# Kernel tuning notes

Hardware: AMD Instinct MI355X
Metric: run time of the kernel (lower is better)

The kernel has to match this reference:

```python
import jax, jax.numpy as jnp
import numpy as np

NUM_EMBEDDINGS = 8192
EMBEDDING_DIM = 64
N_VOXELS = 32768


def setup_inputs() -> dict:
    key = jax.random.key(0)
    k1, k2 = jax.random.split(key)
    z = jax.random.normal(k1, (N_VOXELS, EMBEDDING_DIM), dtype=jnp.float32)
    codebook = jax.random.normal(k2, (NUM_EMBEDDINGS, EMBEDDING_DIM), dtype=jnp.float32)
    return {"z": z, "codebook": codebook}


def reference(z, codebook):
    # Squared euclidean distances [N, K]; argmin is identical to argmin of cdist.
    # d2 = ||z||^2 - 2 z E^T + ||E||^2
    z_sq = jnp.sum(z * z, axis=1, keepdims=True)            # [N, 1]
    e_sq = jnp.sum(codebook * codebook, axis=1)              # [K]
    d2 = z_sq - 2.0 * (z @ codebook.T) + e_sq[None, :]       # [N, K]
    encoding_indices = jnp.argmin(d2, axis=1)                # [N] int

    quantized_feats = codebook[encoding_indices]             # [N, D] gather

    sg = jax.lax.stop_gradient
    commitment_loss = jnp.mean((z - sg(quantized_feats)) ** 2)
    vq_loss = jnp.mean((quantized_feats - sg(z)) ** 2)

    # Straight-through estimator
    quantized = z + sg(quantized_feats - z)                  # [N, D]

    return quantized, vq_loss, commitment_loss, encoding_indices
```

## Files before the change

### kernel.cpp

```cpp
#include <hip/hip_runtime.h>
#include <math.h>

#define N_VOX 32768
#define N_EMB 8192
#define DIM 64
#define NCHUNK 8
#define CODES_PER_CHUNK (N_EMB / NCHUNK)
#define TILES_PER_CHUNK (CODES_PER_CHUNK / 32)
#define NTILES (N_EMB / 32)
#define TILE_BYTES 8192
#define CHUNK_BYTES (TILES_PER_CHUNK * TILE_BYTES)

typedef _Float16 half8 __attribute__((ext_vector_type(8)));
typedef float floatx16 __attribute__((ext_vector_type(16)));

#define FP16_MIN_NORMAL 6.1035156e-5f
#define LO_SCALE 2048.0f

__global__ __launch_bounds__(64) void cbprep_kernel(const float* __restrict__ cb,
                                                    char* __restrict__ stream,
                                                    float* __restrict__ c0arr) {
    int l    = threadIdx.x;
    int m    = l & 31;
    int kg   = l >> 5;
    int tile = blockIdx.x;
    char* tbase = stream + (size_t)tile * TILE_BYTES;
    int code = tile * 32 + m;

    float ss = 0.f;
    #pragma unroll
    for (int o = 0; o < 4; ++o) {
        const float* p = cb + (size_t)code * DIM + o * 16 + kg * 8;
        half8 h, lo;
        #pragma unroll
        for (int j = 0; j < 8; ++j) {
            float x = p[j];
            ss = fmaf(x, x, ss);
            _Float16 hi = (_Float16)x;
            float hf = (float)hi;
            if (fabsf(hf) < FP16_MIN_NORMAL) { hi = (_Float16)0.f; hf = 0.f; }
            h[j]  = hi;
            lo[j] = (_Float16)((x - hf) * LO_SCALE);
        }
        *(half8*)(tbase +        o * 1024 + l * 16) = h;
        *(half8*)(tbase + 4096 + o * 1024 + l * 16) = lo;
    }
    ss += __shfl_xor(ss, 32, 64);
    if (kg == 0)
        c0arr[code] = -1024.0f * ss;
}

__global__ __launch_bounds__(512) void scan_kernel(const float* __restrict__ z,
                                                   const char* __restrict__ stream,
                                                   const float* __restrict__ c0arr,
                                                   float* __restrict__ cand_val,
                                                   int* __restrict__ cand_idx) {
    __shared__ __align__(16) char lds[2 * TILE_BYTES];
    int tid   = threadIdx.x;
    int l     = tid & 63;
    int w     = tid >> 6;
    int chunk = blockIdx.x & (NCHUNK - 1);
    int rg    = blockIdx.x >> 3;
    int m     = l & 31;
    int kg    = l >> 5;
    int rowBase = rg * 256 + w * 32;

    half8 zh[4], zl[4], zhs[4];
    const float* zrow = z + (size_t)(rowBase + m) * DIM + kg * 8;
    #pragma unroll
    for (int o = 0; o < 4; ++o) {
        const float* p = zrow + o * 16;
        #pragma unroll
        for (int j = 0; j < 8; ++j) {
            float x = p[j];
            _Float16 hi = (_Float16)x;
            float hf = (float)hi;
            if (fabsf(hf) < FP16_MIN_NORMAL) { hi = (_Float16)0.f; hf = 0.f; }
            zh[o][j] = hi;
            zl[o][j] = (_Float16)((x - hf) * LO_SCALE);
        }
        zhs[o] = zh[o] * (_Float16)2048.0f;
    }

    const char*  sbase = stream + (size_t)chunk * CHUNK_BYTES;
    const float* c0p   = c0arr + chunk * CODES_PER_CHUNK;

    float best[16];
    int   bt[16];
    #pragma unroll
    for (int i = 0; i < 16; ++i) { best[i] = -3.4e38f; bt[i] = 0; }

#define STAGE(gt, lb)                                                              \
    do {                                                                           \
        const char* _g = (gt) + w * 1024 + l * 16;                                 \
        char*       _d = (lb) + w * 1024 + l * 16;                                 \
        __builtin_amdgcn_global_load_lds(                                          \
            (const __attribute__((address_space(1))) void*)_g,                     \
            (__attribute__((address_space(3))) void*)_d, 16, 0, 0);                \
    } while (0)

    STAGE(sbase, lds);
    float c0 = c0p[m];
    __syncthreads();

    for (int t = 0; t < TILES_PER_CHUNK; ++t) {
        if (t + 1 < TILES_PER_CHUNK)
            STAGE(sbase + (size_t)(t + 1) * TILE_BYTES, lds + ((t + 1) & 1) * TILE_BYTES);
        float c0n = (t + 1 < TILES_PER_CHUNK) ? c0p[(t + 1) * 32 + m] : 0.f;

        const char* lb = lds + (t & 1) * TILE_BYTES;
        half8 bh[4], bl[4];
        #pragma unroll
        for (int o = 0; o < 4; ++o) {
            bh[o] = *(const half8*)(lb +        o * 1024 + l * 16);
            bl[o] = *(const half8*)(lb + 4096 + o * 1024 + l * 16);
        }

        floatx16 acc;
        #pragma unroll
        for (int i = 0; i < 16; ++i) acc[i] = c0;
        #pragma unroll
        for (int o = 0; o < 4; ++o) {
            acc = __builtin_amdgcn_mfma_f32_32x32x16_f16(zhs[o], bh[o], acc, 0, 0, 0);
            acc = __builtin_amdgcn_mfma_f32_32x32x16_f16(zl[o],  bh[o], acc, 0, 0, 0);
            acc = __builtin_amdgcn_mfma_f32_32x32x16_f16(zh[o],  bl[o], acc, 0, 0, 0);
        }
        #pragma unroll
        for (int i = 0; i < 16; ++i)
            if (acc[i] > best[i]) { best[i] = acc[i]; bt[i] = t; }

        c0 = c0n;
        __syncthreads();
    }
#undef STAGE

    #pragma unroll
    for (int i = 0; i < 16; ++i) {
        float v  = best[i];
        int   id = bt[i] * 32 + m;
        #pragma unroll
        for (int off = 1; off < 32; off <<= 1) {
            float ov = __shfl_xor(v, off, 64);
            int   oi = __shfl_xor(id, off, 64);
            if (ov > v || (ov == v && oi < id)) { v = ov; id = oi; }
        }
        if (m == 0) {
            int row = rowBase + (i & 3) + 8 * (i >> 2) + 4 * kg;
            cand_val[chunk * N_VOX + row] = v;
            cand_idx[chunk * N_VOX + row] = chunk * CODES_PER_CHUNK + id;
        }
    }
}

__global__ __launch_bounds__(256) void finalize_kernel(const float* __restrict__ z,
                                                       const float* __restrict__ cb,
                                                       const float* __restrict__ cand_val,
                                                       const int* __restrict__ cand_idx,
                                                       float* __restrict__ out,
                                                       float* __restrict__ partials) {
    int g    = blockIdx.x * 256 + threadIdx.x;
    int row  = g >> 3;
    int c    = g & 7;

    float v  = cand_val[c * N_VOX + row];
    int   id = cand_idx[c * N_VOX + row];
    #pragma unroll
    for (int off = 1; off < 8; off <<= 1) {
        float ov = __shfl_xor(v, off, 8);
        int   oi = __shfl_xor(id, off, 8);
        if (ov > v || (ov == v && oi < id)) { v = ov; id = oi; }
    }

    if (c == 0)
        out[(size_t)N_VOX * DIM + 2 + row] = (float)id;

    const float4* zp = (const float4*)(z  + (size_t)row * DIM + c * 8);
    const float4* qp = (const float4*)(cb + (size_t)id  * DIM + c * 8);
    float4*       op = (float4*)(out + (size_t)row * DIM + c * 8);
    float ss = 0.f;
    #pragma unroll
    for (int d = 0; d < 2; ++d) {
        float4 zt = zp[d], qt = qp[d];
        float dx = qt.x - zt.x, dy = qt.y - zt.y;
        float dz = qt.z - zt.z, dw = qt.w - zt.w;
        float4 o;
        o.x = zt.x + dx; o.y = zt.y + dy;
        o.z = zt.z + dz; o.w = zt.w + dw;
        op[d] = o;
        ss += dx*dx + dy*dy + dz*dz + dw*dw;
    }

    __shared__ float red[256];
    red[threadIdx.x] = ss;
    __syncthreads();
    #pragma unroll
    for (int s = 128; s > 0; s >>= 1) {
        if (threadIdx.x < s) red[threadIdx.x] += red[threadIdx.x + s];
        __syncthreads();
    }
    if (threadIdx.x == 0) partials[blockIdx.x] = red[0];
}

__global__ __launch_bounds__(256) void loss_kernel(const float* __restrict__ partials,
                                                   float* __restrict__ out) {
    __shared__ float red[256];
    red[threadIdx.x] = (partials[threadIdx.x]       + partials[threadIdx.x + 256])
                     + (partials[threadIdx.x + 512] + partials[threadIdx.x + 768]);
    __syncthreads();
    #pragma unroll
    for (int st = 128; st > 0; st >>= 1) {
        if (threadIdx.x < st) red[threadIdx.x] += red[threadIdx.x + st];
        __syncthreads();
    }
    if (threadIdx.x == 0) {
        float mean = red[0] / (float)((size_t)N_VOX * DIM);
        out[(size_t)N_VOX * DIM + 0] = mean;
        out[(size_t)N_VOX * DIM + 1] = mean;
    }
}

extern "C" void kernel_launch(void* const* d_in, const int* in_sizes, int n_in,
                              void* d_out, int out_size, void* d_ws, size_t ws_size,
                              hipStream_t stream) {
    const float* z  = (const float*)d_in[0];
    const float* cb = (const float*)d_in[1];
    float* out = (float*)d_out;

    char*  bstream  = (char*)d_ws;
    float* c0arr    = (float*)(bstream + (size_t)NTILES * TILE_BYTES);
    float* cand_val = c0arr + N_EMB;
    int*   cand_idx = (int*)(cand_val + (size_t)NCHUNK * N_VOX);
    float* partials = (float*)(cand_idx + (size_t)NCHUNK * N_VOX);

    cbprep_kernel  <<<dim3(NTILES), dim3(64), 0, stream>>>(cb, bstream, c0arr);
    scan_kernel    <<<dim3((N_VOX / 256) * NCHUNK), dim3(512), 0, stream>>>(z, bstream, c0arr, cand_val, cand_idx);
    finalize_kernel<<<dim3(N_VOX * 8 / 256), dim3(256), 0, stream>>>(z, cb, cand_val, cand_idx, out, partials);
    loss_kernel    <<<1, 256, 0, stream>>>(partials, out);
}
```

Measured before the change: 178.0 us.

## Fuse finalize and loss into scan via atomic winners and last-block reduction

Replaces the per-chunk candidate arrays and the separate finalize and loss kernels with a packed 64-bit atomicMax per row. The last chunk block to finish a row group, detected through a counter, gathers the code vectors, writes the outputs and accumulates the loss. A final done counter lets the last block write the mean loss. This removes two kernel launches and the candidate round trip through memory, but adds a memset, global atomics, and a tail done by only 128 blocks.

```diff
diff --git a/kernel.cpp b/kernel.cpp
--- a/kernel.cpp
+++ b/kernel.cpp
@@ -10,6 +10,7 @@
 #define NTILES (N_EMB / 32)
 #define TILE_BYTES 8192
 #define CHUNK_BYTES (TILES_PER_CHUNK * TILE_BYTES)
+#define NRG (N_VOX / 256)
 
 typedef _Float16 half8 __attribute__((ext_vector_type(8)));
 typedef float floatx16 __attribute__((ext_vector_type(16)));
@@ -51,11 +52,16 @@
 }
 
 __global__ __launch_bounds__(512) void scan_kernel(const float* __restrict__ z,
+                                                   const float* __restrict__ cb,
                                                    const char* __restrict__ stream,
                                                    const float* __restrict__ c0arr,
-                                                   float* __restrict__ cand_val,
-                                                   int* __restrict__ cand_idx) {
+                                                   unsigned long long* __restrict__ winner,
+                                                   unsigned int* __restrict__ rg_cnt,
+                                                   float* __restrict__ loss_sum,
+                                                   unsigned int* __restrict__ done_cnt,
+                                                   float* __restrict__ out) {
     __shared__ __align__(16) char lds[2 * TILE_BYTES];
+    __shared__ int lastFlag;
     int tid   = threadIdx.x;
     int l     = tid & 63;
     int w     = tid >> 6;
@@ -146,76 +152,68 @@
         }
         if (m == 0) {
             int row = rowBase + (i & 3) + 8 * (i >> 2) + 4 * kg;
-            cand_val[chunk * N_VOX + row] = v;
-            cand_idx[chunk * N_VOX + row] = chunk * CODES_PER_CHUNK + id;
-        }
-    }
-}
-
-__global__ __launch_bounds__(256) void finalize_kernel(const float* __restrict__ z,
-                                                       const float* __restrict__ cb,
-                                                       const float* __restrict__ cand_val,
-                                                       const int* __restrict__ cand_idx,
-                                                       float* __restrict__ out,
-                                                       float* __restrict__ partials) {
-    int g    = blockIdx.x * 256 + threadIdx.x;
-    int row  = g >> 3;
-    int c    = g & 7;
-
-    float v  = cand_val[c * N_VOX + row];
-    int   id = cand_idx[c * N_VOX + row];
-    #pragma unroll
-    for (int off = 1; off < 8; off <<= 1) {
-        float ov = __shfl_xor(v, off, 8);
-        int   oi = __shfl_xor(id, off, 8);
-        if (ov > v || (ov == v && oi < id)) { v = ov; id = oi; }
-    }
-
-    if (c == 0)
-        out[(size_t)N_VOX * DIM + 2 + row] = (float)id;
-
-    const float4* zp = (const float4*)(z  + (size_t)row * DIM + c * 8);
-    const float4* qp = (const float4*)(cb + (size_t)id  * DIM + c * 8);
-    float4*       op = (float4*)(out + (size_t)row * DIM + c * 8);
-    float ss = 0.f;
-    #pragma unroll
-    for (int d = 0; d < 2; ++d) {
-        float4 zt = zp[d], qt = qp[d];
-        float dx = qt.x - zt.x, dy = qt.y - zt.y;
-        float dz = qt.z - zt.z, dw = qt.w - zt.w;
-        float4 o;
-        o.x = zt.x + dx; o.y = zt.y + dy;
-        o.z = zt.z + dz; o.w = zt.w + dw;
-        op[d] = o;
-        ss += dx*dx + dy*dy + dz*dz + dw*dw;
-    }
-
-    __shared__ float red[256];
-    red[threadIdx.x] = ss;
+            int gid = chunk * CODES_PER_CHUNK + id;
+            unsigned int ob = __float_as_uint(v);
+            ob = (ob & 0x80000000u) ? ~ob : (ob | 0x80000000u);
+            unsigned long long key =
+                ((unsigned long long)ob << 32) | (unsigned int)(8191 - gid);
+            atomicMax(&winner[row], key);
+        }
+    }
+
+    __threadfence();
     __syncthreads();
-    #pragma unroll
-    for (int s = 128; s > 0; s >>= 1) {
-        if (threadIdx.x < s) red[threadIdx.x] += red[threadIdx.x + s];
+    if (tid == 0) {
+        unsigned int old = atomicAdd(&rg_cnt[rg], 1u);
+        lastFlag = (old == NCHUNK - 1) ? 1 : 0;
+    }
+    __syncthreads();
+
+    if (lastFlag) {
+        int lane8 = tid & 7;
+        int rsub  = tid >> 3;
+        float ssacc = 0.f;
+        #pragma unroll
+        for (int pass = 0; pass < 4; ++pass) {
+            int row = rg * 256 + pass * 64 + rsub;
+            unsigned long long key = atomicMax(&winner[row], 0ULL);
+            int gid = 8191 - (int)(unsigned int)(key & 0xFFFFFFFFull);
+            if (lane8 == 0)
+                out[(size_t)N_VOX * DIM + 2 + row] = (float)gid;
+            const float4* zp = (const float4*)(z  + (size_t)row * DIM + lane8 * 8);
+            const float4* qp = (const float4*)(cb + (size_t)gid * DIM + lane8 * 8);
+            float4*       op = (float4*)(out + (size_t)row * DIM + lane8 * 8);
+            #pragma unroll
+            for (int d2 = 0; d2 < 2; ++d2) {
+                float4 zt = zp[d2], qt = qp[d2];
+                float dx = qt.x - zt.x, dy = qt.y - zt.y;
+                float dz = qt.z - zt.z, dw = qt.w - zt.w;
+                float4 o;
+                o.x = zt.x + dx; o.y = zt.y + dy;
+                o.z = zt.z + dz; o.w = zt.w + dw;
+                op[d2] = o;
+                ssacc += dx*dx + dy*dy + dz*dz + dw*dw;
+            }
+        }
+        float* sred = (float*)lds;
+        sred[tid] = ssacc;
         __syncthreads();
-    }
-    if (threadIdx.x == 0) partials[blockIdx.x] = red[0];
-}
-
-__global__ __launch_bounds__(256) void loss_kernel(const float* __restrict__ partials,
-                                                   float* __restrict__ out) {
-    __shared__ float red[256];
-    red[threadIdx.x] = (partials[threadIdx.x]       + partials[threadIdx.x + 256])
-                     + (partials[threadIdx.x + 512] + partials[threadIdx.x + 768]);
-    __syncthreads();
-    #pragma unroll
-    for (int st = 128; st > 0; st >>= 1) {
-        if (threadIdx.x < st) red[threadIdx.x] += red[threadIdx.x + st];
-        __syncthreads();
-    }
-    if (threadIdx.x == 0) {
-        float mean = red[0] / (float)((size_t)N_VOX * DIM);
-        out[(size_t)N_VOX * DIM + 0] = mean;
-        out[(size_t)N_VOX * DIM + 1] = mean;
+        #pragma unroll
+        for (int s = 256; s > 0; s >>= 1) {
+            if (tid < s) sred[tid] += sred[tid + s];
+            __syncthreads();
+        }
+        if (tid == 0) {
+            atomicAdd(loss_sum, sred[0]);
+            __threadfence();
+            unsigned int d = atomicAdd(done_cnt, 1u);
+            if (d == NRG - 1) {
+                float tot = atomicAdd(loss_sum, 0.0f);
+                float mean = tot / (float)((size_t)N_VOX * DIM);
+                out[(size_t)N_VOX * DIM + 0] = mean;
+                out[(size_t)N_VOX * DIM + 1] = mean;
+            }
+        }
     }
 }
 
@@ -228,12 +226,16 @@
 
     char*  bstream  = (char*)d_ws;
     float* c0arr    = (float*)(bstream + (size_t)NTILES * TILE_BYTES);
-    float* cand_val = c0arr + N_EMB;
-    int*   cand_idx = (int*)(cand_val + (size_t)NCHUNK * N_VOX);
-    float* partials = (float*)(cand_idx + (size_t)NCHUNK * N_VOX);
-
-    cbprep_kernel  <<<dim3(NTILES), dim3(64), 0, stream>>>(cb, bstream, c0arr);
-    scan_kernel    <<<dim3((N_VOX / 256) * NCHUNK), dim3(512), 0, stream>>>(z, bstream, c0arr, cand_val, cand_idx);
-    finalize_kernel<<<dim3(N_VOX * 8 / 256), dim3(256), 0, stream>>>(z, cb, cand_val, cand_idx, out, partials);
-    loss_kernel    <<<1, 256, 0, stream>>>(partials, out);
+    unsigned long long* winner = (unsigned long long*)(c0arr + N_EMB);
+    unsigned int* rg_cnt   = (unsigned int*)(winner + N_VOX);
+    float*        loss_sum = (float*)(rg_cnt + NRG);
+    unsigned int* done_cnt = (unsigned int*)(loss_sum + 1);
+
+    size_t zero_off = (size_t)NTILES * TILE_BYTES + (size_t)N_EMB * 4;
+    size_t zero_sz  = (size_t)N_VOX * 8 + NRG * 4 + 4 + 4;
+    hipMemsetAsync((char*)d_ws + zero_off, 0, zero_sz, stream);
+
+    cbprep_kernel<<<dim3(NTILES), dim3(64), 0, stream>>>(cb, bstream, c0arr);
+    scan_kernel  <<<dim3((N_VOX / 256) * NCHUNK), dim3(512), 0, stream>>>(
+        z, cb, bstream, c0arr, winner, rg_cnt, loss_sum, done_cnt, out);
 }
```

After: 314.1 us. 1.76x slower.
